# Kernel tuning notes

Measured on AMD Instinct MI355X. Metric: run time of the kernel, lower is better.

## Reference

```python
import jax, jax.numpy as jnp
import numpy as np

N = 256            # state_space_size
BF = (4, 4, 4)     # branching_factors
T = 128            # time steps
D_IN = 64          # input_size
D_T = 64           # time_embedding_size
BATCH = 16
NUM_NODES = N * 4 * 4 * 4  # 16384


def setup_inputs() -> dict:
    key = jax.random.key(0)
    ks = jax.random.split(key, 20)

    def lin_w(k, out_d, in_d):
        return jax.random.normal(k, (out_d, in_d), jnp.float32) / np.sqrt(in_d)

    inp = {
        "x": jax.random.normal(ks[0], (BATCH, T, N), jnp.float32),
        "t_embeddings_schedule": jax.random.normal(ks[1], (T, D_T), jnp.float32),
        "input_vector": jax.random.normal(ks[2], (BATCH, T, D_IN), jnp.float32),
        # Fanout node params
        "Wa": lin_w(ks[3], NUM_NODES, N),
        "ba": jnp.zeros((NUM_NODES,), jnp.float32),
        "Wt": lin_w(ks[4], NUM_NODES, D_T),
        "Wi": lin_w(ks[5], NUM_NODES, D_IN),
        # Node with bf[:3]=[4,4,4]: reduces last 4 -> [N,4,4]
        "w3": jax.random.normal(ks[6], (N, 4, 4, 4), jnp.float32) * np.sqrt(2.0 / (4 + N * 16)),
        "tW3": lin_w(ks[7], N * 16, D_T),
        "tb3": jnp.zeros((N * 16,), jnp.float32),
        # Node with bf[:2]=[4,4]
        "w2": jax.random.normal(ks[8], (N, 4, 4), jnp.float32) * np.sqrt(2.0 / (4 + N * 4)),
        "tW2": lin_w(ks[9], N * 4, D_T),
        "tb2": jnp.zeros((N * 4,), jnp.float32),
        # Node with bf[:1]=[4]
        "w1": jax.random.normal(ks[10], (N, 4), jnp.float32) * np.sqrt(2.0 / (4 + N)),
        "tW1": lin_w(ks[11], N, D_T),
        "tb1": jnp.zeros((N,), jnp.float32),
    }
    return inp


def _node(act, t_emb, w, tW, tb):
    # act: [..., T, N, *bf]; w: [N, *bf]; reduce last branching dim
    tproj = (t_emb @ tW.T + tb).reshape(t_emb.shape[0], *w.shape[:-1])  # [T, N, *bf[:-1]]
    pre = (w * act).sum(-1) + tproj  # broadcast over leading batch dims
    return jax.nn.softplus(pre)


def reference(x, t_embeddings_schedule, input_vector, Wa, ba, Wt, Wi,
              w3, tW3, tb3, w2, tW2, tb2, w1, tW1, tb1):
    t_emb = t_embeddings_schedule
    # Fanout: [B, T, N] -> [B, T, N, 4, 4, 4]
    pre = x @ Wa.T + ba + (t_emb @ Wt.T) + input_vector @ Wi.T  # [B, T, NUM_NODES]
    act = jax.nn.softplus(pre.reshape(*pre.shape[:-1], N, *BF))
    # Tree: deepest node first (insert-at-1 order in original)
    act = _node(act, t_emb, w3, tW3, tb3)  # [B, T, N, 4, 4]
    act = _node(act, t_emb, w2, tW2, tb2)  # [B, T, N, 4]
    act = _node(act, t_emb, w1, tW1, tb1)  # [B, T, N]
    return act
```

## Files before the change

### kernel.cpp

```cpp
#include <hip/hip_runtime.h>

typedef __attribute__((ext_vector_type(16))) float f32x16;
typedef __attribute__((ext_vector_type(8))) __bf16 bf16x8;
typedef __attribute__((ext_vector_type(8))) unsigned short u16x8;

__device__ __forceinline__ unsigned short f2bf(float f) {
    unsigned int u = __float_as_uint(f);
    u += 0x7fffu + ((u >> 16) & 1u);
    return (unsigned short)(u >> 16);
}

__device__ __forceinline__ float softplus_f(float x) {
    float e = __expf(-fabsf(x));
    return fmaxf(x, 0.0f) + __logf(1.0f + e);
}

typedef __attribute__((address_space(3))) void lds_void_t;
typedef __attribute__((address_space(1))) void glb_void_t;

__device__ __forceinline__ void load16_to_lds(const void* g, const void* l) {
    __builtin_amdgcn_global_load_lds((glb_void_t*)(unsigned long long)g,
                                     (lds_void_t*)(unsigned int)(unsigned long long)l,
                                     16, 0, 0);
}

#define REPACK_NB 2
#define REPACK_BLOCKS 1728
__global__ __launch_bounds__(256) void repack(
        const float* __restrict__ x, const float* __restrict__ iv,
        const float* __restrict__ temb,
        const float* __restrict__ Wa, const float* __restrict__ Wi,
        const float* __restrict__ Wt,
        unsigned short* __restrict__ Abf ) {
    const int stride = REPACK_BLOCKS * 256;
    const int tid0 = blockIdx.x * 256 + threadIdx.x;
    float4 f[REPACK_NB][2];
    #pragma unroll
    for (int c = 0; c < REPACK_NB; ++c) {
        const int idx = tid0 + c * stride;
        const bool isA = idx < 98304;
        const int widx = isA ? idx : idx - 98304;
        const int row = widx / 48;
        const int kk  = (widx % 48) * 8;
        const float* p0 = isA ? (x    + (size_t)row * 256) : (Wa + (size_t)row * 256);
        const float* p1 = isA ? (iv   + (size_t)row * 64)  : (Wi + (size_t)row * 64);
        const float* p2 = isA ? (temb + (size_t)(row & 127) * 64) : (Wt + (size_t)row * 64);
        const float* src = (kk < 256) ? (p0 + kk) : ((kk < 320) ? (p1 + kk - 256) : (p2 + kk - 320));
        f[c][0] = ((const float4*)src)[0];
        f[c][1] = ((const float4*)src)[1];
    }
    #pragma unroll
    for (int c = 0; c < REPACK_NB; ++c) {
        const int idx = tid0 + c * stride;
        u16x8 o;
        o[0] = f2bf(f[c][0].x); o[1] = f2bf(f[c][0].y); o[2] = f2bf(f[c][0].z); o[3] = f2bf(f[c][0].w);
        o[4] = f2bf(f[c][1].x); o[5] = f2bf(f[c][1].y); o[6] = f2bf(f[c][1].z); o[7] = f2bf(f[c][1].w);
        *(u16x8*)(Abf + (size_t)idx * 8) = o;
    }
}

__global__ __launch_bounds__(256) void tproj(
        const float* __restrict__ temb,
        const float* __restrict__ tW3, const float* __restrict__ tb3,
        const float* __restrict__ tW2, const float* __restrict__ tb2,
        const float* __restrict__ tW1, const float* __restrict__ tb1,
        float* __restrict__ tp3T, float* __restrict__ tp2T, float* __restrict__ tp1T) {
    __shared__ float se[32 * 64];
    const int tid = threadIdx.x;
    const int tbase = blockIdx.y * 32;
    for (int i = tid; i < 32 * 64; i += 256) se[i] = temb[tbase * 64 + i];
    __syncthreads();
    const int j = blockIdx.x * 64 + (tid >> 2);
    const float* W; const float* bias; float* outp; int jl;
    if      (j < 4096) { W = tW3; bias = tb3; outp = tp3T; jl = j; }
    else if (j < 5120) { W = tW2; bias = tb2; outp = tp2T; jl = j - 4096; }
    else               { W = tW1; bias = tb1; outp = tp1T; jl = j - 5120; }
    float4 wreg[16];
    const float4* wrow = (const float4*)(W + (size_t)jl * 64);
    #pragma unroll
    for (int k = 0; k < 16; ++k) wreg[k] = wrow[k];
    const float b = bias[jl];
    #pragma unroll
    for (int s = 0; s < 8; ++s) {
        const int tl = (tid & 3) + s * 4;
        const float4* e4 = (const float4*)&se[tl * 64];
        float a = b;
        #pragma unroll
        for (int k = 0; k < 16; ++k) {
            float4 e = e4[k];
            a += wreg[k].x * e.x + wreg[k].y * e.y + wreg[k].z * e.z + wreg[k].w * e.w;
        }
        outp[(size_t)jl * 128 + tbase + tl] = a;
    }
}

__global__ __launch_bounds__(256, 4)
void fused_gemm_tree(const unsigned short* __restrict__ Wbf,
                     const unsigned short* __restrict__ Abf,
                     const float* __restrict__ ba,
                     const float* __restrict__ tp3T, const float* __restrict__ tp2T,
                     const float* __restrict__ tp1T,
                     const float* __restrict__ w3, const float* __restrict__ w2,
                     const float* __restrict__ w1,
                     float* __restrict__ out) {
    __shared__ unsigned short sW[128 * 64];
    __shared__ unsigned short sA[128 * 64];

    const int tid  = threadIdx.x;
    const int wave = tid >> 6;
    const int lane = tid & 63;
    const int wr = wave >> 1;
    const int wc = wave & 1;
    const int lane31 = lane & 31;
    const int h = lane >> 5;

    const int node0 = blockIdx.x * 128;
    const int m0    = blockIdx.y * 128;

    f32x16 acc[2][2];
    #pragma unroll
    for (int fm = 0; fm < 2; ++fm)
        #pragma unroll
        for (int s2 = 0; s2 < 4; ++s2) {
            const float4 b4 = *(const float4*)&ba[node0 + wr * 64 + fm * 32 + 8 * s2 + 4 * h];
            #pragma unroll
            for (int l = 0; l < 4; ++l) {
                acc[fm][0][s2 * 4 + l] = ((const float*)&b4)[l];
                acc[fm][1][s2 * 4 + l] = ((const float*)&b4)[l];
            }
        }

    const unsigned short* aBase = Wbf + (size_t)node0 * 384;
    const unsigned short* bBase = Abf + (size_t)m0 * 384;

    const int wrow0 = wr * 64 + lane31;
    const int arow0 = wc * 64 + lane31;

    for (int k0 = 0; k0 < 384; k0 += 64) {
        __syncthreads();
        #pragma unroll
        for (int rr = 0; rr < 4; ++rr) {
            const int p = rr * 256 + tid;
            const int row = p >> 3;
            const int kchunk = (p & 7) ^ (row & 7);
            const size_t soff = (size_t)row * 384 + k0 + kchunk * 8;
            load16_to_lds(aBase + soff, &sW[(size_t)(rr * 256 + wave * 64) * 8]);
            load16_to_lds(bBase + soff, &sA[(size_t)(rr * 256 + wave * 64) * 8]);
        }
        __syncthreads();

        #pragma unroll
        for (int s = 0; s < 4; ++s) {
            const int kc = s * 2 + h;
            bf16x8 af[2], bf[2];
            #pragma unroll
            for (int fm = 0; fm < 2; ++fm) {
                const int row = wrow0 + fm * 32;
                af[fm] = *(const bf16x8*)&sW[row * 64 + (kc ^ (row & 7)) * 8];
            }
            #pragma unroll
            for (int cf = 0; cf < 2; ++cf) {
                const int row = arow0 + cf * 32;
                bf[cf] = *(const bf16x8*)&sA[row * 64 + (kc ^ (row & 7)) * 8];
            }
            #pragma unroll
            for (int fm = 0; fm < 2; ++fm)
                #pragma unroll
                for (int cf = 0; cf < 2; ++cf)
                    acc[fm][cf] = __builtin_amdgcn_mfma_f32_32x32x16_bf16(af[fm], bf[cf], acc[fm][cf], 0, 0, 0);
        }
    }

    const int n = blockIdx.x * 2 + wr;
    const int t0 = wc * 64 + lane31;

    float4 w3v[2][4];
    #pragma unroll
    for (int fm = 0; fm < 2; ++fm)
        #pragma unroll
        for (int s2 = 0; s2 < 4; ++s2)
            w3v[fm][s2] = *(const float4*)&w3[n * 64 + fm * 32 + 8 * s2 + 4 * h];

    float w2v[4][2], w1v[4];
    #pragma unroll
    for (int i = 0; i < 4; ++i) {
        #pragma unroll
        for (int s2b = 0; s2b < 2; ++s2b)
            w2v[i][s2b] = w2[n * 16 + i * 4 + 2 * s2b + h];
        w1v[i] = w1[n * 4 + i];
    }
    float tp3v[2][2][4];
    #pragma unroll
    for (int fm = 0; fm < 2; ++fm)
        #pragma unroll
        for (int cf = 0; cf < 2; ++cf) {
            const int t = t0 + cf * 32;
            #pragma unroll
            for (int s2 = 0; s2 < 4; ++s2) {
                const int i  = fm * 2 + (s2 >> 1);
                const int jj = 2 * (s2 & 1) + h;
                tp3v[fm][cf][s2] = tp3T[(size_t)((n * 4 + i) * 4 + jj) * 128 + t];
            }
        }
    const int th = t0 + h * 32;
    float tp2h[2][2];
    #pragma unroll
    for (int fm = 0; fm < 2; ++fm)
        #pragma unroll
        for (int b = 0; b < 2; ++b)
            tp2h[fm][b] = tp2T[(size_t)(n * 4 + fm * 2 + b) * 128 + th];
    const float tp1h = tp1T[(size_t)n * 128 + th];

    float s1h = 0.0f;
    #pragma unroll
    for (int fm = 0; fm < 2; ++fm) {
        #pragma unroll
        for (int b = 0; b < 2; ++b) {
            float cs[2];
            #pragma unroll
            for (int cf = 0; cf < 2; ++cf) {
                float c = 0.0f;
                #pragma unroll
                for (int s2b = 0; s2b < 2; ++s2b) {
                    const int s2 = 2 * b + s2b;
                    float p3 = 0.0f;
                    const float* wv = (const float*)&w3v[fm][s2];
                    #pragma unroll
                    for (int l = 0; l < 4; ++l) {
                        float a0 = softplus_f(acc[fm][cf][s2 * 4 + l]);
                        p3 = fmaf(a0, wv[l], p3);
                    }
                    float a3 = softplus_f(p3 + tp3v[fm][cf][s2]);
                    c = fmaf(a3, w2v[fm * 2 + b][s2b], c);
                }
                cs[cf] = c;
            }
            const float Q0 = cs[0] + __shfl_xor(cs[0], 32);
            const float Q1 = cs[1] + __shfl_xor(cs[1], 32);
            const float Qh = h ? Q1 : Q0;
            const float a2 = softplus_f(Qh + tp2h[fm][b]);
            s1h = fmaf(a2, w1v[fm * 2 + b], s1h);
        }
    }
    out[(size_t)(m0 + th) * 256 + n] = softplus_f(s1h + tp1h);
}

extern "C" void kernel_launch(void* const* d_in, const int* in_sizes, int n_in,
                              void* d_out, int out_size, void* d_ws, size_t ws_size,
                              hipStream_t stream) {
    const float* x    = (const float*)d_in[0];
    const float* temb = (const float*)d_in[1];
    const float* iv   = (const float*)d_in[2];
    const float* Wa   = (const float*)d_in[3];
    const float* ba   = (const float*)d_in[4];
    const float* Wt   = (const float*)d_in[5];
    const float* Wi   = (const float*)d_in[6];
    const float* w3   = (const float*)d_in[7];
    const float* tW3  = (const float*)d_in[8];
    const float* tb3  = (const float*)d_in[9];
    const float* w2   = (const float*)d_in[10];
    const float* tW2  = (const float*)d_in[11];
    const float* tb2  = (const float*)d_in[12];
    const float* w1   = (const float*)d_in[13];
    const float* tW1  = (const float*)d_in[14];
    const float* tb1  = (const float*)d_in[15];
    float* out = (float*)d_out;

    char* ws = (char*)d_ws;
    unsigned short* Abf = (unsigned short*)(ws);
    unsigned short* Wbf = (unsigned short*)(ws + 1572864);
    float* tp3T = (float*)(ws + 14155776);
    float* tp2T = (float*)(ws + 16252928);
    float* tp1T = (float*)(ws + 16777216);

    repack<<<dim3(REPACK_BLOCKS), dim3(256), 0, stream>>>(x, iv, temb, Wa, Wi, Wt, Abf);
    tproj<<<dim3(84, 4), dim3(256), 0, stream>>>(temb, tW3, tb3, tW2, tb2, tW1, tb1,
                                                 tp3T, tp2T, tp1T);
    fused_gemm_tree<<<dim3(128, 16), dim3(256), 0, stream>>>(Wbf, Abf, ba, tp3T, tp2T, tp1T,
                                                             w3, w2, w1, out);
}
```

Before: 155.5 us.

## Load activation B-fragments directly from global to registers, drop LDS staging

The activation (B) operand of the fused GEMM is no longer staged through shared memory. Each lane now loads its bf16x8 fragments straight from global memory into registers, which halves LDS usage and removes the LDS reads for B. Each B row is now fetched separately by the two waves that share it instead of once per block, and more registers are needed, so the occupancy hint drops from 4 to 3 blocks. Softplus also switches to log2 scaled by ln2.

```diff
diff --git a/kernel.cpp b/kernel.cpp
--- a/kernel.cpp
+++ b/kernel.cpp
@@ -12,7 +12,7 @@
 
 __device__ __forceinline__ float softplus_f(float x) {
     float e = __expf(-fabsf(x));
-    return fmaxf(x, 0.0f) + __logf(1.0f + e);
+    return fmaf(__log2f(1.0f + e), 0.69314718056f, fmaxf(x, 0.0f));
 }
 
 typedef __attribute__((address_space(3))) void lds_void_t;
@@ -94,7 +94,7 @@
     }
 }
 
-__global__ __launch_bounds__(256, 4)
+__global__ __launch_bounds__(256, 3)
 void fused_gemm_tree(const unsigned short* __restrict__ Wbf,
                      const unsigned short* __restrict__ Abf,
                      const float* __restrict__ ba,
@@ -104,7 +104,6 @@
                      const float* __restrict__ w1,
                      float* __restrict__ out) {
     __shared__ unsigned short sW[128 * 64];
-    __shared__ unsigned short sA[128 * 64];
 
     const int tid  = threadIdx.x;
     const int wave = tid >> 6;
@@ -131,10 +130,11 @@
         }
 
     const unsigned short* aBase = Wbf + (size_t)node0 * 384;
-    const unsigned short* bBase = Abf + (size_t)m0 * 384;
 
     const int wrow0 = wr * 64 + lane31;
     const int arow0 = wc * 64 + lane31;
+    const unsigned short* bptr0 = Abf + (size_t)(m0 + arow0) * 384;
+    const unsigned short* bptr1 = Abf + (size_t)(m0 + arow0 + 32) * 384;
 
     for (int k0 = 0; k0 < 384; k0 += 64) {
         __syncthreads();
@@ -143,31 +143,31 @@
             const int p = rr * 256 + tid;
             const int row = p >> 3;
             const int kchunk = (p & 7) ^ (row & 7);
-            const size_t soff = (size_t)row * 384 + k0 + kchunk * 8;
-            load16_to_lds(aBase + soff, &sW[(size_t)(rr * 256 + wave * 64) * 8]);
-            load16_to_lds(bBase + soff, &sA[(size_t)(rr * 256 + wave * 64) * 8]);
+            load16_to_lds(aBase + (size_t)row * 384 + k0 + kchunk * 8,
+                          &sW[(size_t)(rr * 256 + wave * 64) * 8]);
+        }
+        bf16x8 bfr[2][4];
+        #pragma unroll
+        for (int s = 0; s < 4; ++s) {
+            const int ko = k0 + (s * 2 + h) * 8;
+            bfr[0][s] = *(const bf16x8*)(bptr0 + ko);
+            bfr[1][s] = *(const bf16x8*)(bptr1 + ko);
         }
         __syncthreads();
 
         #pragma unroll
         for (int s = 0; s < 4; ++s) {
             const int kc = s * 2 + h;
-            bf16x8 af[2], bf[2];
-            #pragma unroll
-            for (int fm = 0; fm < 2; ++fm) {
-                const int row = wrow0 + fm * 32;
-                af[fm] = *(const bf16x8*)&sW[row * 64 + (kc ^ (row & 7)) * 8];
-            }
-            #pragma unroll
-            for (int cf = 0; cf < 2; ++cf) {
-                const int row = arow0 + cf * 32;
-                bf[cf] = *(const bf16x8*)&sA[row * 64 + (kc ^ (row & 7)) * 8];
-            }
+            const int slot = (kc ^ (lane31 & 7)) * 8;
+            bf16x8 af[2];
+            #pragma unroll
+            for (int fm = 0; fm < 2; ++fm)
+                af[fm] = *(const bf16x8*)&sW[(wrow0 + fm * 32) * 64 + slot];
             #pragma unroll
             for (int fm = 0; fm < 2; ++fm)
                 #pragma unroll
                 for (int cf = 0; cf < 2; ++cf)
-                    acc[fm][cf] = __builtin_amdgcn_mfma_f32_32x32x16_bf16(af[fm], bf[cf], acc[fm][cf], 0, 0, 0);
+                    acc[fm][cf] = __builtin_amdgcn_mfma_f32_32x32x16_bf16(af[fm], bfr[cf][s], acc[fm][cf], 0, 0, 0);
         }
     }
 
```

Result: slower. 177.5 us (+14.2%).
